# Kernel optimization log

Hardware: AMD Instinct MI355X
Metric: run time of the kernel (lower is better)

## Reference

```python
import jax, jax.numpy as jnp
import numpy as np
import math

EMBED_DIM = 1024
NUM_HEADS = 16
HEAD_DIM = EMBED_DIM // NUM_HEADS


def setup_inputs() -> dict:
    key = jax.random.key(0)
    ks = jax.random.split(key, 5)
    x = jax.random.normal(ks[0], (4, 2048, EMBED_DIM), dtype=jnp.float32)
    # Linear params (torch nn.Linear: y = x @ W.T + b); init scale ~ 1/sqrt(fan_in)
    s = 1.0 / math.sqrt(EMBED_DIM)
    qkv_w = jax.random.uniform(ks[1], (3 * EMBED_DIM, EMBED_DIM), jnp.float32, -s, s)
    qkv_b = jax.random.uniform(ks[2], (3 * EMBED_DIM,), jnp.float32, -s, s)
    proj_w = jax.random.uniform(ks[3], (EMBED_DIM, EMBED_DIM), jnp.float32, -s, s)
    proj_b = jax.random.uniform(ks[4], (EMBED_DIM,), jnp.float32, -s, s)
    return {"x": x, "qkv_w": qkv_w, "qkv_b": qkv_b, "proj_w": proj_w, "proj_b": proj_b}


def reference(x, qkv_w, qkv_b, proj_w, proj_b):
    bsz, num_tokens, dim = x.shape
    qkv = x @ qkv_w.T + qkv_b  # [B, S, 3*D]
    qkv = qkv.reshape(bsz, num_tokens, 3, NUM_HEADS, HEAD_DIM)
    qkv = jnp.transpose(qkv, (2, 0, 3, 1, 4))  # [3, B, H, S, hd]
    q, k, v = qkv[0], qkv[1], qkv[2]
    scale = 1.0 / math.sqrt(HEAD_DIM)
    attn_scores = jnp.einsum('bhqd,bhkd->bhqk', q, k) * scale  # [B, H, S, S]
    attn = jax.nn.softmax(attn_scores, axis=-1)
    out = jnp.einsum('bhqk,bhkd->bhqd', attn, v)  # [B, H, S, hd]
    out = jnp.transpose(out, (0, 2, 1, 3)).reshape(bsz, num_tokens, dim)
    out = out @ proj_w.T + proj_b
    return out
```

## Files before the change

### kernel.cpp

```cpp
#include <hip/hip_runtime.h>
#include <stdint.h>

#define DEVICE static __device__ __forceinline__

typedef __bf16 bf16x8 __attribute__((ext_vector_type(8)));
typedef float f32x4 __attribute__((ext_vector_type(4)));

#define AS1 __attribute__((address_space(1)))
#define AS3 __attribute__((address_space(3)))

DEVICE void g2l16(const void* gptr, void* lptr) {
  __builtin_amdgcn_global_load_lds((AS1 uint32_t*)(uintptr_t)gptr,
                                   (AS3 uint32_t*)(uint32_t)(uintptr_t)lptr,
                                   16, 0, 0);
}

DEVICE float b2f(ushort h) {
  union { uint32_t u; float f; } v;
  v.u = ((uint32_t)h) << 16;
  return v.f;
}
DEVICE ushort f2b(float f) {
  union { float f; uint32_t u; } v;
  v.f = f;
  uint32_t u = v.u;
  return (ushort)((u + 0x7FFFu + ((u >> 16) & 1u)) >> 16);
}

#if defined(__has_builtin) && __has_builtin(__builtin_amdgcn_exp2f)
DEVICE float fast_exp2(float x) { return __builtin_amdgcn_exp2f(x); }
#else
extern "C" __device__ float __ocml_native_exp2_f32(float);
DEVICE float fast_exp2(float x) { return __ocml_native_exp2_f32(x); }
#endif

#define QSCALE 0.1803368801111244f

DEVICE int kperm(int x) {
  return (x & 0x23) | ((x & 0x18) >> 1) | ((x & 0x4) << 2);
}

__global__ void detect_dtype(const ushort* __restrict__ xu, int* __restrict__ flag) {
  __shared__ int bad;
  if (threadIdx.x == 0) bad = 0;
  __syncthreads();
  int mybad = 0;
#pragma unroll
  for (int j = 0; j < 8; ++j) {
    const int i = threadIdx.x * 8 + j;
    const ushort u = xu[2 * i];
    const int e = (u >> 7) & 0xFF;
    if (!(e == 0 || (e >= 96 && e <= 160))) mybad++;
  }
  atomicAdd(&bad, mybad);
  __syncthreads();
  if (threadIdx.x == 0) *flag = (bad > 512) ? 1 : 0;
}

__global__ void convert_all(const void* __restrict__ s0, const void* __restrict__ s1,
                            const void* __restrict__ s2, const void* __restrict__ s3,
                            const void* __restrict__ s4,
                            ushort* __restrict__ d0, ushort* __restrict__ d1,
                            ushort* __restrict__ d2, ushort* __restrict__ d3,
                            ushort* __restrict__ d4,
                            const int* __restrict__ flag) {
  const bool isf32 = (*flag != 0);
  for (int g = blockIdx.x * blockDim.x + threadIdx.x; g < 1573376;
       g += gridDim.x * blockDim.x) {
    const void* src; ushort* dst; int i;
    if (g < 1048576)      { src = s0; dst = d0; i = g; }
    else if (g < 1441792) { src = s1; dst = d1; i = g - 1048576; }
    else if (g < 1442176) { src = s2; dst = d2; i = g - 1441792; }
    else if (g < 1573248) { src = s3; dst = d3; i = g - 1442176; }
    else                  { src = s4; dst = d4; i = g - 1573248; }
    ushort pk[8];
    if (isf32) {
      const float4 a = ((const float4*)src)[2 * i];
      const float4 b = ((const float4*)src)[2 * i + 1];
      pk[0] = f2b(a.x); pk[1] = f2b(a.y); pk[2] = f2b(a.z); pk[3] = f2b(a.w);
      pk[4] = f2b(b.x); pk[5] = f2b(b.y); pk[6] = f2b(b.z); pk[7] = f2b(b.w);
      *(uint4*)&dst[8 * i] = *(const uint4*)pk;
    } else {
      *(uint4*)&dst[8 * i] = ((const uint4*)src)[i];
    }
  }
}

template <int MODE, int GN, int MT>
__global__ __launch_bounds__(512, 4)
void gemm256(const ushort* __restrict__ A, const ushort* __restrict__ W,
             const ushort* __restrict__ bias, ushort* __restrict__ O0,
             ushort* __restrict__ O1, ushort* __restrict__ O2,
             int M, int N, int K, const int* __restrict__ flag)
{
  constexpr int BM = MT * 32;
  constexpr int ABYTES = BM * 64;
  constexpr int BUFB = ABYTES + 16384;
  constexpr int SMEMB = (MODE == 0) ? 49152 : 2 * BUFB;
  __shared__ __align__(16) char smem[SMEMB];

  const int tid = threadIdx.x;
  const int lane = tid & 63;
  const int wave = tid >> 6;
  const int quad = lane >> 4;
  const int lo = lane & 15;

  const int lin = blockIdx.y * gridDim.x + blockIdx.x;
  const int per = GN * gridDim.y;
  const int grp = lin / per;
  const int w   = lin % per;
  const int bxn = grp * GN + (w % GN);
  const int bym = w / GN;
  const int m0 = bym * BM;
  const int n0 = bxn * 256;

  const int wm = (wave >> 2) * (MT * 16);
  const int wn = (wave & 3) * 64;

  const int rA = tid >> 2;
  const int gA = (tid & 3) << 3;
  const size_t offA  = (size_t)(m0 + rA) * K + gA;
  const size_t offB0 = (size_t)(n0 + rA) * K + gA;
  const size_t offB1 = (size_t)(n0 + 128 + rA) * K + gA;
  const int dA = wave << 10;
  const bool aload = (MT == 4) || (tid < 256);
  const int NT = K >> 5;

  f32x4 acc[MT][4];
#pragma unroll
  for (int mt = 0; mt < MT; ++mt)
#pragma unroll
    for (int nt = 0; nt < 4; ++nt) acc[mt][nt] = (f32x4){0.f, 0.f, 0.f, 0.f};

  if (aload) g2l16(A + offA, smem + dA);
  g2l16(W + offB0, smem + ABYTES + dA);
  g2l16(W + offB1, smem + ABYTES + 8192 + dA);
  asm volatile("s_waitcnt vmcnt(0)" ::: "memory");
  __builtin_amdgcn_s_barrier();

  for (int kt = 0; kt < NT; ++kt) {
    const char* buf = smem + (kt & 1) * BUFB;
    const ushort* Al = (const ushort*)buf;
    const ushort* Bl = (const ushort*)(buf + ABYTES);
    const bool pf = (kt + 1 < NT);
    char* nbuf = smem + ((kt + 1) & 1) * BUFB;
    const size_t nk = (size_t)(kt + 1) * 32;

    if (pf) {
      if (aload) g2l16(A + offA + nk, nbuf + dA);
      g2l16(W + offB0 + nk, nbuf + ABYTES + dA);
    }
    bf16x8 bfr[4], af[MT / 2];
#pragma unroll
    for (int nt = 0; nt < 4; ++nt)
      bfr[nt] = *(const bf16x8*)&Bl[(wn + nt * 16 + lo) * 32 + quad * 8];
#pragma unroll
    for (int mt = 0; mt < MT / 2; ++mt)
      af[mt] = *(const bf16x8*)&Al[(wm + mt * 16 + lo) * 32 + quad * 8];
    __builtin_amdgcn_s_setprio(1);
#pragma unroll
    for (int mt = 0; mt < MT / 2; ++mt)
#pragma unroll
      for (int nt = 0; nt < 4; ++nt)
        acc[mt][nt] = __builtin_amdgcn_mfma_f32_16x16x32_bf16(
            af[mt], bfr[nt], acc[mt][nt], 0, 0, 0);
    __builtin_amdgcn_s_setprio(0);
    __builtin_amdgcn_s_barrier();

    if (pf)
      g2l16(W + offB1 + nk, nbuf + ABYTES + 8192 + dA);
    bf16x8 af2[MT / 2];
#pragma unroll
    for (int mt = 0; mt < MT / 2; ++mt)
      af2[mt] = *(const bf16x8*)&Al[(wm + (mt + MT / 2) * 16 + lo) * 32 + quad * 8];
    __builtin_amdgcn_s_setprio(1);
#pragma unroll
    for (int mt = 0; mt < MT / 2; ++mt)
#pragma unroll
      for (int nt = 0; nt < 4; ++nt)
        acc[mt + MT / 2][nt] = __builtin_amdgcn_mfma_f32_16x16x32_bf16(
            af2[mt], bfr[nt], acc[mt + MT / 2][nt], 0, 0, 0);
    __builtin_amdgcn_s_setprio(0);

    if (kt < NT - 1) {
      asm volatile("s_waitcnt vmcnt(0)" ::: "memory");
      __builtin_amdgcn_s_barrier();
    }
  }

  if (MODE == 0) {
    const int which = n0 >> 10;
    if (which == 2) {
#pragma unroll
      for (int nt = 0; nt < 4; ++nt) {
        const int n = n0 + wn + nt * 16 + lo;
        const float bv = b2f(bias[n]);
        const int h = (n >> 6) & 15;
        const int d = n & 63;
#pragma unroll
        for (int mt = 0; mt < MT; ++mt) {
          const int m = m0 + wm + mt * 16 + quad * 4;
          const int b = m >> 11, s0 = m & 2047;
          ushort pk[4];
#pragma unroll
          for (int r = 0; r < 4; ++r) pk[r] = f2b(acc[mt][nt][r] + bv);
          *(uint2*)&O2[((size_t)(b * 16 + h) * 64 + d) * 2048 + s0] =
              *(const uint2*)pk;
        }
      }
    } else {
      const float qs = (which == 0) ? QSCALE : 1.0f;
      ushort* __restrict__ dst = (which == 0) ? O0 : O1;
      const int h = ((n0 + wn) >> 6) & 15;
      __syncthreads();
      ushort* scr = (ushort*)(smem + wave * 5632);
      float bv[4];
#pragma unroll
      for (int nt = 0; nt < 4; ++nt) bv[nt] = b2f(bias[n0 + wn + nt * 16 + lo]);
#pragma unroll
      for (int c2 = 0; c2 < MT / 2; ++c2) {
#pragma unroll
        for (int mtl = 0; mtl < 2; ++mtl)
#pragma unroll
          for (int nt = 0; nt < 4; ++nt)
#pragma unroll
            for (int r = 0; r < 4; ++r)
              scr[(mtl * 16 + quad * 4 + r) * 88 + nt * 16 + lo] =
                  f2b((acc[c2 * 2 + mtl][nt][r] + bv[nt]) * qs);
        asm volatile("s_waitcnt lgkmcnt(0)" ::: "memory");
#pragma unroll
        for (int i = 0; i < 4; ++i) {
          const int id = lane + 64 * i;
          const int rowl = id >> 3, nch = id & 7;
          const uint4 val = *(const uint4*)&scr[rowl * 88 + nch * 8];
          const int m = m0 + wm + c2 * 32 + rowl;
          const int b = m >> 11;
          int s = m & 2047;
          if (which == 1) s = (s & ~63) | kperm(s & 63);
          *(uint4*)&dst[((size_t)(b * 16 + h) * 2048 + s) * 64 + nch * 8] = val;
        }
      }
    }
  } else {
    const bool f32out = (*flag != 0);
    float* Of = (float*)O0;
#pragma unroll
    for (int nt = 0; nt < 4; ++nt) {
      const int n = n0 + wn + nt * 16 + lo;
      const float bv = b2f(bias[n]);
#pragma unroll
      for (int mt = 0; mt < MT; ++mt)
#pragma unroll
        for (int r = 0; r < 4; ++r) {
          const int m = m0 + wm + mt * 16 + quad * 4 + r;
          const float val = acc[mt][nt][r] + bv;
          if (f32out) Of[(size_t)m * N + n] = val;
          else        O0[(size_t)m * N + n] = f2b(val);
        }
    }
  }
}

__global__ __launch_bounds__(256, 4)
void attn_fwd(const ushort* __restrict__ qp, const ushort* __restrict__ kp,
              const ushort* __restrict__ vp, ushort* __restrict__ o)
{
  __shared__ ushort SA[128 * 64];
  __shared__ ushort SB[2][64 * 64];

  const int tid = threadIdx.x;
  const int lane = tid & 63;
  const int wave = tid >> 6;
  const int quad = lane >> 4;
  const int lo = lane & 15;
  const int sw = (lo & 7) << 3;

  const int lin = blockIdx.y * gridDim.x + blockIdx.x;
  const int bh = (lin & 7) * 8 + ((lin >> 3) & 7);
  const int q0 = (lin >> 6) * 128;

  const ushort* Qg = qp + (size_t)bh * 2048 * 64;
  const ushort* Kg = kp + (size_t)bh * 2048 * 64;
  const ushort* Vg = vp + (size_t)bh * 64 * 2048;

#pragma unroll
  for (int i = 0; i < 4; ++i) {
    const int c = tid + 256 * i;
    const int row = c >> 3;
    const int kc = ((c ^ row) & 7) << 3;
    g2l16(Qg + (size_t)(q0 + row) * 64 + kc,
          (char*)SA + ((wave << 6) + (i << 8)) * 16);
  }
#pragma unroll
  for (int i = 0; i < 2; ++i) {
    const int c = tid + 256 * i;
    const int row = c >> 3;
    const int kc = ((c ^ row) & 7) << 3;
    g2l16(Kg + (size_t)row * 64 + kc,
          (char*)SB[0] + ((wave << 6) + (i << 8)) * 16);
    g2l16(Vg + (size_t)row * 2048 + kc,
          (char*)SB[1] + ((wave << 6) + (i << 8)) * 16);
  }
  asm volatile("s_waitcnt vmcnt(0)" ::: "memory");
  __builtin_amdgcn_s_barrier();

  bf16x8 qf[2][2];
#pragma unroll
  for (int mt = 0; mt < 2; ++mt)
#pragma unroll
    for (int ks = 0; ks < 2; ++ks)
      qf[mt][ks] = *(const bf16x8*)&SA[(wave * 32 + mt * 16 + lo) * 64 +
                                       ((ks * 32 + quad * 8) ^ sw)];

  __syncthreads();

  bf16x8 ones;
#pragma unroll
  for (int j = 0; j < 8; ++j) ones[j] = (__bf16)1.0f;

  f32x4 oacc[2][4] = {};
  f32x4 sumacc[2] = {};

  for (int t = 0; t < 32; ++t) {
    const int cur = t & 1;
    const ushort* Kc = cur ? SA : SB[0];
    const ushort* Vc = cur ? (SA + 64 * 64) : SB[1];
    char* Kn = (char*)(cur ? SB[0] : SA);
    char* Vn = (char*)(cur ? SB[1] : (SA + 64 * 64));

    if (t < 31) {
      const int j1 = (t + 1) * 64;
#pragma unroll
      for (int i = 0; i < 2; ++i) {
        const int c = tid + 256 * i;
        const int row = c >> 3;
        const int kc = ((c ^ row) & 7) << 3;
        g2l16(Kg + (size_t)(j1 + row) * 64 + kc,
              Kn + ((wave << 6) + (i << 8)) * 16);
        g2l16(Vg + (size_t)row * 2048 + j1 + kc,
              Vn + ((wave << 6) + (i << 8)) * 16);
      }
    }

    f32x4 sacc[2][4] = {};
#pragma unroll
    for (int ks = 0; ks < 2; ++ks) {
#pragma unroll
      for (int nt = 0; nt < 4; ++nt) {
        const bf16x8 kf =
            *(const bf16x8*)&Kc[(nt * 16 + lo) * 64 + ((ks * 32 + quad * 8) ^ sw)];
#pragma unroll
        for (int mt = 0; mt < 2; ++mt)
          sacc[mt][nt] = __builtin_amdgcn_mfma_f32_16x16x32_bf16(
              kf, qf[mt][ks], sacc[mt][nt], 0, 0, 0);
      }
    }

    bf16x8 pfr[2][2];
#pragma unroll
    for (int mt = 0; mt < 2; ++mt) {
      float p[4][4];
#pragma unroll
      for (int nt = 0; nt < 4; ++nt)
#pragma unroll
        for (int r = 0; r < 4; ++r)
          p[nt][r] = fast_exp2(sacc[mt][nt][r]);
#pragma unroll
      for (int b = 0; b < 2; ++b)
#pragma unroll
        for (int h = 0; h < 2; ++h)
#pragma unroll
          for (int r = 0; r < 4; ++r)
            pfr[mt][b][4 * h + r] = (__bf16)p[2 * b + h][r];
    }

#pragma unroll
    for (int b = 0; b < 2; ++b) {
#pragma unroll
      for (int mt = 0; mt < 2; ++mt)
        sumacc[mt] = __builtin_amdgcn_mfma_f32_16x16x32_bf16(
            pfr[mt][b], ones, sumacc[mt], 0, 0, 0);
#pragma unroll
      for (int dt = 0; dt < 4; ++dt) {
        const bf16x8 vf =
            *(const bf16x8*)&Vc[(dt * 16 + lo) * 64 + ((b * 32 + quad * 8) ^ sw)];
#pragma unroll
        for (int mt = 0; mt < 2; ++mt)
          oacc[mt][dt] = __builtin_amdgcn_mfma_f32_16x16x32_bf16(
              pfr[mt][b], vf, oacc[mt][dt], 0, 0, 0);
      }
    }

    asm volatile("s_waitcnt vmcnt(0)" ::: "memory");
    __builtin_amdgcn_s_barrier();
  }

  const int b_ = bh >> 4;
  const int h = bh & 15;
#pragma unroll
  for (int mt = 0; mt < 2; ++mt) {
#pragma unroll
    for (int r = 0; r < 4; ++r) {
      const float inv = 1.0f / sumacc[mt][r];
      const int srow = q0 + wave * 32 + mt * 16 + quad * 4 + r;
#pragma unroll
      for (int dt = 0; dt < 4; ++dt) {
        o[(((size_t)(b_ * 2048 + srow)) << 10) + h * 64 + dt * 16 + lo] =
            f2b(oacc[mt][dt][r] * inv);
      }
    }
  }
}

extern "C" void kernel_launch(void* const* d_in, const int* in_sizes, int n_in,
                              void* d_out, int out_size, void* d_ws, size_t ws_size,
                              hipStream_t stream) {
  const size_t N_X  = (size_t)4 * 2048 * 1024;
  const size_t N_WQ = (size_t)3072 * 1024;
  const size_t N_BQ = 3072;
  const size_t N_WP = (size_t)1024 * 1024;
  const size_t N_BP = 1024;
  const size_t HSD  = (size_t)64 * 2048 * 64;

  ushort* xb = (ushort*)d_ws;
  ushort* wq = xb + N_X;
  ushort* bq = wq + N_WQ;
  ushort* wp = bq + N_BQ;
  ushort* bp = wp + N_WP;
  ushort* qb = bp + N_BP;
  ushort* kb = qb + HSD;
  ushort* vb = kb + HSD;
  ushort* ab = vb + HSD;
  int* flag  = (int*)(ab + HSD);

  detect_dtype<<<1, 256, 0, stream>>>((const ushort*)d_in[0], flag);
  convert_all<<<2048, 256, 0, stream>>>(d_in[0], d_in[1], d_in[2], d_in[3], d_in[4],
                                        xb, wq, bq, wp, bp, flag);

  gemm256<0, 4, 4><<<dim3(12, 64), dim3(512), 0, stream>>>(
      xb, wq, bq, qb, kb, vb, 8192, 3072, 1024, flag);
  attn_fwd<<<dim3(16, 64), dim3(256), 0, stream>>>(qb, kb, vb, ab);
  gemm256<1, 4, 2><<<dim3(4, 128), dim3(512), 0, stream>>>(
      ab, wp, bp, (ushort*)d_out, nullptr, nullptr, 8192, 1024, 1024, flag);
}
```

Before: 271.0 us.

## Load GEMM A fragments directly from global into registers, stage only W in LDS

The GEMM no longer stages the A tile through shared memory. Each lane reads its A fragments straight from global memory into registers, double-buffered across two unrolled k-steps, and only the weight tile goes through LDS. This removes A's LDS traffic and shrinks shared memory to 32 KB for non-QKV modes, which could allow more blocks per CU. In exchange, A reads are uncoalesced and strided by K, A data is no longer shared between waves, and more registers are needed.

```diff
diff --git a/kernel.cpp b/kernel.cpp
--- a/kernel.cpp
+++ b/kernel.cpp
@@ -93,10 +93,7 @@
              ushort* __restrict__ O1, ushort* __restrict__ O2,
              int M, int N, int K, const int* __restrict__ flag)
 {
-  constexpr int BM = MT * 32;
-  constexpr int ABYTES = BM * 64;
-  constexpr int BUFB = ABYTES + 16384;
-  constexpr int SMEMB = (MODE == 0) ? 49152 : 2 * BUFB;
+  constexpr int SMEMB = (MODE == 0) ? 49152 : 32768;
   __shared__ __align__(16) char smem[SMEMB];
 
   const int tid = threadIdx.x;
@@ -111,80 +108,108 @@
   const int w   = lin % per;
   const int bxn = grp * GN + (w % GN);
   const int bym = w / GN;
-  const int m0 = bym * BM;
+  const int m0 = bym * (MT * 32);
   const int n0 = bxn * 256;
 
   const int wm = (wave >> 2) * (MT * 16);
   const int wn = (wave & 3) * 64;
 
-  const int rA = tid >> 2;
-  const int gA = (tid & 3) << 3;
-  const size_t offA  = (size_t)(m0 + rA) * K + gA;
-  const size_t offB0 = (size_t)(n0 + rA) * K + gA;
-  const size_t offB1 = (size_t)(n0 + 128 + rA) * K + gA;
+  const int rB = tid >> 2;
+  const int gB = (tid & 3) << 3;
+  const size_t offB0 = (size_t)(n0 + rB) * K + gB;
+  const size_t offB1 = (size_t)(n0 + 128 + rB) * K + gB;
   const int dA = wave << 10;
-  const bool aload = (MT == 4) || (tid < 256);
   const int NT = K >> 5;
 
+  const ushort* Ag = A + (size_t)(m0 + wm + lo) * K + (quad << 3);
+
   f32x4 acc[MT][4];
 #pragma unroll
   for (int mt = 0; mt < MT; ++mt)
 #pragma unroll
     for (int nt = 0; nt < 4; ++nt) acc[mt][nt] = (f32x4){0.f, 0.f, 0.f, 0.f};
 
-  if (aload) g2l16(A + offA, smem + dA);
-  g2l16(W + offB0, smem + ABYTES + dA);
-  g2l16(W + offB1, smem + ABYTES + 8192 + dA);
+  bf16x8 afA[MT], afB[MT];
+
+#pragma unroll
+  for (int mt = 0; mt < MT; ++mt)
+    afA[mt] = *(const bf16x8*)(Ag + (size_t)(mt * 16) * K);
+  g2l16(W + offB0, smem + dA);
+  g2l16(W + offB1, smem + 8192 + dA);
   asm volatile("s_waitcnt vmcnt(0)" ::: "memory");
   __builtin_amdgcn_s_barrier();
 
-  for (int kt = 0; kt < NT; ++kt) {
-    const char* buf = smem + (kt & 1) * BUFB;
-    const ushort* Al = (const ushort*)buf;
-    const ushort* Bl = (const ushort*)(buf + ABYTES);
-    const bool pf = (kt + 1 < NT);
-    char* nbuf = smem + ((kt + 1) & 1) * BUFB;
-    const size_t nk = (size_t)(kt + 1) * 32;
-
-    if (pf) {
-      if (aload) g2l16(A + offA + nk, nbuf + dA);
-      g2l16(W + offB0 + nk, nbuf + ABYTES + dA);
-    }
-    bf16x8 bfr[4], af[MT / 2];
-#pragma unroll
-    for (int nt = 0; nt < 4; ++nt)
-      bfr[nt] = *(const bf16x8*)&Bl[(wn + nt * 16 + lo) * 32 + quad * 8];
-#pragma unroll
-    for (int mt = 0; mt < MT / 2; ++mt)
-      af[mt] = *(const bf16x8*)&Al[(wm + mt * 16 + lo) * 32 + quad * 8];
-    __builtin_amdgcn_s_setprio(1);
-#pragma unroll
-    for (int mt = 0; mt < MT / 2; ++mt)
+  for (int kt = 0; kt < NT; kt += 2) {
+    {
+      const ushort* Bl = (const ushort*)smem;
+      char* nbuf = smem + 16384;
+      const size_t nk = (size_t)(kt + 1) * 32;
+#pragma unroll
+      for (int mt = 0; mt < MT; ++mt)
+        afB[mt] = *(const bf16x8*)(Ag + (size_t)(mt * 16) * K + nk);
+      g2l16(W + offB0 + nk, nbuf + dA);
+      g2l16(W + offB1 + nk, nbuf + 8192 + dA);
+      bf16x8 bfr[4];
 #pragma unroll
       for (int nt = 0; nt < 4; ++nt)
-        acc[mt][nt] = __builtin_amdgcn_mfma_f32_16x16x32_bf16(
-            af[mt], bfr[nt], acc[mt][nt], 0, 0, 0);
-    __builtin_amdgcn_s_setprio(0);
-    __builtin_amdgcn_s_barrier();
-
-    if (pf)
-      g2l16(W + offB1 + nk, nbuf + ABYTES + 8192 + dA);
-    bf16x8 af2[MT / 2];
-#pragma unroll
-    for (int mt = 0; mt < MT / 2; ++mt)
-      af2[mt] = *(const bf16x8*)&Al[(wm + (mt + MT / 2) * 16 + lo) * 32 + quad * 8];
-    __builtin_amdgcn_s_setprio(1);
-#pragma unroll
-    for (int mt = 0; mt < MT / 2; ++mt)
-#pragma unroll
-      for (int nt = 0; nt < 4; ++nt)
-        acc[mt + MT / 2][nt] = __builtin_amdgcn_mfma_f32_16x16x32_bf16(
-            af2[mt], bfr[nt], acc[mt + MT / 2][nt], 0, 0, 0);
-    __builtin_amdgcn_s_setprio(0);
-
-    if (kt < NT - 1) {
+        bfr[nt] = *(const bf16x8*)&Bl[(wn + nt * 16 + lo) * 32 + quad * 8];
+      __builtin_amdgcn_s_setprio(1);
+#pragma unroll
+      for (int mt = 0; mt < MT / 2; ++mt)
+#pragma unroll
+        for (int nt = 0; nt < 4; ++nt)
+          acc[mt][nt] = __builtin_amdgcn_mfma_f32_16x16x32_bf16(
+              afA[mt], bfr[nt], acc[mt][nt], 0, 0, 0);
+      __builtin_amdgcn_s_setprio(0);
+      __builtin_amdgcn_s_barrier();
+      __builtin_amdgcn_s_setprio(1);
+#pragma unroll
+      for (int mt = MT / 2; mt < MT; ++mt)
+#pragma unroll
+        for (int nt = 0; nt < 4; ++nt)
+          acc[mt][nt] = __builtin_amdgcn_mfma_f32_16x16x32_bf16(
+              afA[mt], bfr[nt], acc[mt][nt], 0, 0, 0);
+      __builtin_amdgcn_s_setprio(0);
       asm volatile("s_waitcnt vmcnt(0)" ::: "memory");
       __builtin_amdgcn_s_barrier();
+    }
+    {
+      const ushort* Bl = (const ushort*)(smem + 16384);
+      char* nbuf = smem;
+      const bool pf = (kt + 2 < NT);
+      const size_t nk = (size_t)(kt + 2) * 32;
+      if (pf) {
+#pragma unroll
+        for (int mt = 0; mt < MT; ++mt)
+          afA[mt] = *(const bf16x8*)(Ag + (size_t)(mt * 16) * K + nk);
+        g2l16(W + offB0 + nk, nbuf + dA);
+        g2l16(W + offB1 + nk, nbuf + 8192 + dA);
+      }
+      bf16x8 bfr[4];
+#pragma unroll
+      for (int nt = 0; nt < 4; ++nt)
+        bfr[nt] = *(const bf16x8*)&Bl[(wn + nt * 16 + lo) * 32 + quad * 8];
+      __builtin_amdgcn_s_setprio(1);
+#pragma unroll
+      for (int mt = 0; mt < MT / 2; ++mt)
+#pragma unroll
+        for (int nt = 0; nt < 4; ++nt)
+          acc[mt][nt] = __builtin_amdgcn_mfma_f32_16x16x32_bf16(
+              afB[mt], bfr[nt], acc[mt][nt], 0, 0, 0);
+      __builtin_amdgcn_s_setprio(0);
+      __builtin_amdgcn_s_barrier();
+      __builtin_amdgcn_s_setprio(1);
+#pragma unroll
+      for (int mt = MT / 2; mt < MT; ++mt)
+#pragma unroll
+        for (int nt = 0; nt < 4; ++nt)
+          acc[mt][nt] = __builtin_amdgcn_mfma_f32_16x16x32_bf16(
+              afB[mt], bfr[nt], acc[mt][nt], 0, 0, 0);
+      __builtin_amdgcn_s_setprio(0);
+      if (pf) {
+        asm volatile("s_waitcnt vmcnt(0)" ::: "memory");
+        __builtin_amdgcn_s_barrier();
+      }
     }
   }
 
```

Result: slower. 388.7 us (+43.4%).
